# Optimization experiments

Hardware: AMD Instinct MI355X
Metric: run time of the kernel (lower is better)

The kernel has to match this reference:

```python
import jax, jax.numpy as jnp
import numpy as np

C_LEN, Q_LEN, B, H = 2048, 512, 32, 256


def setup_inputs() -> dict:
    key = jax.random.key(0)
    k1, k2 = jax.random.split(key)
    content_vec = jax.random.normal(k1, (C_LEN, B, H), dtype=jnp.float32)
    question_vec = jax.random.normal(k2, (Q_LEN, B, H), dtype=jnp.float32)
    question_mask = jnp.ones((B, Q_LEN), dtype=jnp.int32)
    return {"content_vec": content_vec, "question_vec": question_vec, "question_mask": question_mask}


def reference(content_vec, question_vec, question_mask):
    # scores: (B, c_len, q_len) = content (b,c,h) @ question^T (b,h,q)
    scores = jnp.einsum('cbh,qbh->bcq', content_vec, question_vec)
    # additive -inf mask where question_mask == 0, broadcast over c_len
    neg_inf = jnp.asarray(-jnp.inf, dtype=scores.dtype)
    scores = jnp.where(question_mask[:, None, :] == 0, neg_inf, scores)
    attn = jax.nn.softmax(scores, axis=-1)  # (B, c_len, q_len)
    # weighted sum of question vectors -> back to (c_len, B, H)
    out = jnp.einsum('bcq,qbh->cbh', attn, question_vec)
    return out
```

## Files before the change

### kernel.cpp

```cpp
#include <hip/hip_runtime.h>

#define C_LENX 2048
#define Q_LENX 512
#define BATCH  32
#define HDIM   256
#define BH     8192
#define CBLK   128
#define QBLK   32
#define NQT    16
#define TILE_BYTES 32768
#define OFF_QT 16384

typedef __attribute__((ext_vector_type(8))) _Float16 f16x8;
typedef __attribute__((ext_vector_type(4))) _Float16 f16x4;
typedef __attribute__((ext_vector_type(4))) float f32x4;

__device__ __forceinline__ unsigned short f2h_bits(float x) {
    union { _Float16 h; unsigned short u; } cv;
    cv.h = (_Float16)x;
    return cv.u;
}

__device__ __forceinline__ void stage16(const void* gsrc, void* ldst) {
    __builtin_amdgcn_global_load_lds(
        (const __attribute__((address_space(1))) unsigned int*)gsrc,
        (__attribute__((address_space(3))) unsigned int*)ldst, 16, 0, 0);
}

__global__ __launch_bounds__(256)
void q_prep(const float* __restrict__ question, unsigned char* __restrict__ blob)
{
    __shared__ unsigned short sHf[QBLK][264];
    const int tid = threadIdx.x;
    const int b  = blockIdx.x >> 4;
    const int t  = blockIdx.x & 15;
    const float* qbase = question + (size_t)(t * QBLK) * BH + b * HDIM;
    unsigned char* tb = blob + (size_t)(b * NQT + t) * TILE_BYTES;

    #pragma unroll
    for (int i = 0; i < 8; ++i) {
        int e  = tid + i * 256;
        int qr = e >> 6;
        int h4 = (e & 63) << 2;
        float4 x = *reinterpret_cast<const float4*>(qbase + (size_t)qr * BH + h4);
        ushort4 hv;
        hv.x = f2h_bits(x.x); hv.y = f2h_bits(x.y);
        hv.z = f2h_bits(x.z); hv.w = f2h_bits(x.w);
        *reinterpret_cast<ushort4*>(&sHf[qr][h4]) = hv;
        int c = h4 >> 3;
        *reinterpret_cast<ushort4*>(tb + qr * 512 + ((c ^ (qr & 7)) << 4) + ((h4 & 7) << 1)) = hv;
    }
    __syncthreads();
    #pragma unroll
    for (int i = 0; i < 4; ++i) {
        int c   = tid + i * 256;
        int n   = c >> 6;
        int hr  = (c >> 2) & 15;
        int lg4 = c & 3;
        int h  = n * 16 + hr;
        int q0 = lg4 * 4;
        ushort4 lo, hi;
        lo.x = sHf[q0 + 0][h]; lo.y = sHf[q0 + 1][h];
        lo.z = sHf[q0 + 2][h]; lo.w = sHf[q0 + 3][h];
        hi.x = sHf[16 + q0 + 0][h]; hi.y = sHf[16 + q0 + 1][h];
        hi.z = sHf[16 + q0 + 2][h]; hi.w = sHf[16 + q0 + 3][h];
        *reinterpret_cast<ushort4*>(tb + OFF_QT + c * 16)     = lo;
        *reinterpret_cast<ushort4*>(tb + OFF_QT + c * 16 + 8) = hi;
    }
}

__global__ __launch_bounds__(256, 2)
void s2s_attn(const float* __restrict__ content,
              const unsigned char* __restrict__ blob,
              const int*   __restrict__ qmask,
              float*       __restrict__ out)
{
    __shared__ __attribute__((aligned(16))) unsigned char sBuf[2 * TILE_BYTES];

    const int tid  = threadIdx.x;
    const int wid  = tid >> 6;
    const int lane = tid & 63;
    const int lr   = lane & 15;
    const int lg   = lane >> 4;

    const int lin = (blockIdx.x & 7) * 64 + (blockIdx.x >> 3);
    const int ct = lin & 15;
    const int b  = lin >> 4;
    const int c0 = ct * CBLK;

    {
        const unsigned char* tb0 = blob + (size_t)(b * NQT) * TILE_BYTES;
        #pragma unroll
        for (int j = 0; j < 8; ++j) {
            int seg = wid * 8 + j;
            stage16(tb0 + seg * 1024 + lane * 16, sBuf + seg * 1024);
        }
    }

    unsigned mwv[NQT];
    #pragma unroll
    for (int t = 0; t < NQT; ++t)
        mwv[t] = (unsigned)__ballot(qmask[b * Q_LENX + t * QBLK + (lane & 31)] != 0);

    f16x8 chi0[8], chi1[8];
    {
        const float* cb0 = content + (size_t)(c0 + wid*16 + lr) * BH + b*HDIM + lg*8;
        const float* cb1 = cb0 + (size_t)64 * BH;
        #pragma unroll
        for (int kc = 0; kc < 8; ++kc) {
            float4 x0 = *reinterpret_cast<const float4*>(cb0 + kc*32);
            float4 x1 = *reinterpret_cast<const float4*>(cb0 + kc*32 + 4);
            float4 y0 = *reinterpret_cast<const float4*>(cb1 + kc*32);
            float4 y1 = *reinterpret_cast<const float4*>(cb1 + kc*32 + 4);
            float xs[8] = {x0.x,x0.y,x0.z,x0.w,x1.x,x1.y,x1.z,x1.w};
            float ys[8] = {y0.x,y0.y,y0.z,y0.w,y1.x,y1.y,y1.z,y1.w};
            #pragma unroll
            for (int j = 0; j < 8; ++j) {
                chi0[kc][j] = (_Float16)xs[j];
                chi1[kc][j] = (_Float16)ys[j];
            }
        }
    }

    f32x4 acc0[16], acc1[16];
    #pragma unroll
    for (int n = 0; n < 16; ++n) {
        f32x4 z = {0.f,0.f,0.f,0.f};
        acc0[n] = z; acc1[n] = z;
    }
    float m_run0 = -INFINITY, m_run1 = -INFINITY;
    float l_run0 = 0.f, l_run1 = 0.f;

    __syncthreads();

    for (int t = 0; t < NQT; ++t) {
        const unsigned char* qf = sBuf + (t & 1) * TILE_BYTES;
        const unsigned char* qt = qf + OFF_QT;

        if (t + 1 < NQT) {
            const unsigned char* tbn = blob + (size_t)(b * NQT + t + 1) * TILE_BYTES;
            unsigned char* db = sBuf + ((t + 1) & 1) * TILE_BYTES;
            #pragma unroll
            for (int j = 0; j < 8; ++j) {
                int seg = wid * 8 + j;
                stage16(tbn + seg * 1024 + lane * 16, db + seg * 1024);
            }
        }
        const unsigned mw = mwv[t];

        f32x4 zz = {0.f,0.f,0.f,0.f};
        f32x4 sA0=zz, sB0=zz, sA1=zz, sB1=zz;
        const unsigned swz = (unsigned)(lr & 7);
        __builtin_amdgcn_s_setprio(1);
        #pragma unroll
        for (int kc = 0; kc < 8; ++kc) {
            unsigned off = (unsigned)((kc*4 + lg) ^ swz) << 4;
            f16x8 qa = *reinterpret_cast<const f16x8*>(qf + lr*512 + off);
            f16x8 qb = *reinterpret_cast<const f16x8*>(qf + (16+lr)*512 + off);
            sA0 = __builtin_amdgcn_mfma_f32_16x16x32_f16(qa, chi0[kc], sA0, 0, 0, 0);
            sB0 = __builtin_amdgcn_mfma_f32_16x16x32_f16(qb, chi0[kc], sB0, 0, 0, 0);
            sA1 = __builtin_amdgcn_mfma_f32_16x16x32_f16(qa, chi1[kc], sA1, 0, 0, 0);
            sB1 = __builtin_amdgcn_mfma_f32_16x16x32_f16(qb, chi1[kc], sB1, 0, 0, 0);
        }
        __builtin_amdgcn_s_setprio(0);

        float p0[8], p1[8];
        float tm0 = -INFINITY, tm1 = -INFINITY;
        #pragma unroll
        for (int r = 0; r < 4; ++r) {
            bool okA = (mw >> (lg*4 + r)) & 1u;
            bool okB = (mw >> (16 + lg*4 + r)) & 1u;
            float a0 = okA ? sA0[r] : -INFINITY;
            float b0v = okB ? sB0[r] : -INFINITY;
            float a1 = okA ? sA1[r] : -INFINITY;
            float b1v = okB ? sB1[r] : -INFINITY;
            p0[r] = a0; p0[4+r] = b0v;
            p1[r] = a1; p1[4+r] = b1v;
            tm0 = fmaxf(tm0, fmaxf(a0, b0v));
            tm1 = fmaxf(tm1, fmaxf(a1, b1v));
        }
        tm0 = fmaxf(tm0, __shfl_xor(tm0, 16, 64));
        tm0 = fmaxf(tm0, __shfl_xor(tm0, 32, 64));
        tm1 = fmaxf(tm1, __shfl_xor(tm1, 16, 64));
        tm1 = fmaxf(tm1, __shfl_xor(tm1, 32, 64));

        if (__ballot((tm0 > m_run0 + 4.0f) || (tm1 > m_run1 + 4.0f))) {
            float mn0 = fmaxf(m_run0, tm0);
            float mn1 = fmaxf(m_run1, tm1);
            float sc0 = 1.f, sc1 = 1.f;
            if (mn0 != -INFINITY) { sc0 = __expf(m_run0 - mn0); m_run0 = mn0; }
            if (mn1 != -INFINITY) { sc1 = __expf(m_run1 - mn1); m_run1 = mn1; }
            l_run0 *= sc0; l_run1 *= sc1;
            #pragma unroll
            for (int n = 0; n < 16; ++n) {
                acc0[n] *= sc0;
                acc1[n] *= sc1;
            }
        }

        _Float16 ph0[8], ph1[8];
        {
            float ps0 = 0.f, ps1 = 0.f;
            if (m_run0 == -INFINITY) {
                #pragma unroll
                for (int i = 0; i < 8; ++i) ph0[i] = (_Float16)0.f;
            } else {
                #pragma unroll
                for (int i = 0; i < 8; ++i) {
                    float e = __expf(p0[i] - m_run0);
                    ph0[i] = (_Float16)e;
                    ps0 += (float)ph0[i];
                }
            }
            if (m_run1 == -INFINITY) {
                #pragma unroll
                for (int i = 0; i < 8; ++i) ph1[i] = (_Float16)0.f;
            } else {
                #pragma unroll
                for (int i = 0; i < 8; ++i) {
                    float e = __expf(p1[i] - m_run1);
                    ph1[i] = (_Float16)e;
                    ps1 += (float)ph1[i];
                }
            }
            l_run0 += ps0;
            l_run1 += ps1;
        }

        f16x4 bp00 = {ph0[0], ph0[1], ph0[2], ph0[3]};
        f16x4 bp01 = {ph0[4], ph0[5], ph0[6], ph0[7]};
        f16x4 bp10 = {ph1[0], ph1[1], ph1[2], ph1[3]};
        f16x4 bp11 = {ph1[4], ph1[5], ph1[6], ph1[7]};
        __builtin_amdgcn_s_setprio(1);
        #pragma unroll
        for (int n = 0; n < 16; ++n) {
            f16x8 vt = *reinterpret_cast<const f16x8*>(qt + (((n*16 + lr)*4 + lg) << 4));
            f16x4 alo = {vt[0], vt[1], vt[2], vt[3]};
            f16x4 ahi = {vt[4], vt[5], vt[6], vt[7]};
            acc0[n] = __builtin_amdgcn_mfma_f32_16x16x16f16(alo, bp00, acc0[n], 0, 0, 0);
            acc1[n] = __builtin_amdgcn_mfma_f32_16x16x16f16(alo, bp10, acc1[n], 0, 0, 0);
            acc0[n] = __builtin_amdgcn_mfma_f32_16x16x16f16(ahi, bp01, acc0[n], 0, 0, 0);
            acc1[n] = __builtin_amdgcn_mfma_f32_16x16x16f16(ahi, bp11, acc1[n], 0, 0, 0);
        }
        __builtin_amdgcn_s_setprio(0);

        __syncthreads();
    }

    l_run0 += __shfl_xor(l_run0, 16, 64);
    l_run0 += __shfl_xor(l_run0, 32, 64);
    l_run1 += __shfl_xor(l_run1, 16, 64);
    l_run1 += __shfl_xor(l_run1, 32, 64);
    float rinv0 = 1.f / l_run0;
    float rinv1 = 1.f / l_run1;
    float* orow0 = out + (size_t)(c0 + wid*16 + lr) * BH + b*HDIM;
    float* orow1 = orow0 + (size_t)64 * BH;
    #pragma unroll
    for (int n = 0; n < 16; ++n) {
        f32x4 v0 = acc0[n] * rinv0;
        f32x4 v1 = acc1[n] * rinv1;
        *reinterpret_cast<f32x4*>(orow0 + n*16 + lg*4) = v0;
        *reinterpret_cast<f32x4*>(orow1 + n*16 + lg*4) = v1;
    }
}

extern "C" void kernel_launch(void* const* d_in, const int* in_sizes, int n_in,
                              void* d_out, int out_size, void* d_ws, size_t ws_size,
                              hipStream_t stream) {
    const float* content  = (const float*)d_in[0];
    const float* question = (const float*)d_in[1];
    const int*   mask     = (const int*)d_in[2];
    float*       out      = (float*)d_out;

    unsigned char* blob = (unsigned char*)d_ws;

    q_prep<<<BATCH * NQT, 256, 0, stream>>>(question, blob);
    s2s_attn<<<C_LENX / CBLK * BATCH, 256, 0, stream>>>(content, blob, mask, out);
}
```

Baseline: 80.72 us.

## Use 16x16x32 MFMA for PV by re-laying P through LDS and repacking Q^T

Repacks the transposed question tile so each lane holds 8 consecutive q values, and writes the softmax probabilities to a small per-wave LDS scratch so they can be reloaded in the matching k=32 layout. This halves the MFMA instruction count in the PV product by replacing pairs of 16x16x16 ops with single 16x16x32 ops. It also adds a fast path that skips per-element mask selects when the whole mask word is set. The cost is extra LDS writes and reads plus a waitcnt barrier on each iteration.

```diff
diff --git a/kernel.cpp b/kernel.cpp
--- a/kernel.cpp
+++ b/kernel.cpp
@@ -53,19 +53,17 @@
     __syncthreads();
     #pragma unroll
     for (int i = 0; i < 4; ++i) {
-        int c   = tid + i * 256;
-        int n   = c >> 6;
-        int hr  = (c >> 2) & 15;
-        int lg4 = c & 3;
-        int h  = n * 16 + hr;
-        int q0 = lg4 * 4;
-        ushort4 lo, hi;
-        lo.x = sHf[q0 + 0][h]; lo.y = sHf[q0 + 1][h];
-        lo.z = sHf[q0 + 2][h]; lo.w = sHf[q0 + 3][h];
-        hi.x = sHf[16 + q0 + 0][h]; hi.y = sHf[16 + q0 + 1][h];
-        hi.z = sHf[16 + q0 + 2][h]; hi.w = sHf[16 + q0 + 3][h];
-        *reinterpret_cast<ushort4*>(tb + OFF_QT + c * 16)     = lo;
-        *reinterpret_cast<ushort4*>(tb + OFF_QT + c * 16 + 8) = hi;
+        int e  = tid + i * 256;
+        int h  = e >> 2;
+        int g  = e & 3;
+        int q0 = g * 8;
+        ushort4 a, bv;
+        a.x  = sHf[q0 + 0][h]; a.y  = sHf[q0 + 1][h];
+        a.z  = sHf[q0 + 2][h]; a.w  = sHf[q0 + 3][h];
+        bv.x = sHf[q0 + 4][h]; bv.y = sHf[q0 + 5][h];
+        bv.z = sHf[q0 + 6][h]; bv.w = sHf[q0 + 7][h];
+        *reinterpret_cast<ushort4*>(tb + OFF_QT + e * 16)     = a;
+        *reinterpret_cast<ushort4*>(tb + OFF_QT + e * 16 + 8) = bv;
     }
 }
 
@@ -76,6 +74,7 @@
               float*       __restrict__ out)
 {
     __shared__ __attribute__((aligned(16))) unsigned char sBuf[2 * TILE_BYTES];
+    __shared__ __attribute__((aligned(16))) unsigned short sP[2][4][16][40];
 
     const int tid  = threadIdx.x;
     const int wid  = tid >> 6;
@@ -164,20 +163,30 @@
         }
         __builtin_amdgcn_s_setprio(0);
 
-        float p0[8], p1[8];
+        float p0v[8], p1v[8];
         float tm0 = -INFINITY, tm1 = -INFINITY;
-        #pragma unroll
-        for (int r = 0; r < 4; ++r) {
-            bool okA = (mw >> (lg*4 + r)) & 1u;
-            bool okB = (mw >> (16 + lg*4 + r)) & 1u;
-            float a0 = okA ? sA0[r] : -INFINITY;
-            float b0v = okB ? sB0[r] : -INFINITY;
-            float a1 = okA ? sA1[r] : -INFINITY;
-            float b1v = okB ? sB1[r] : -INFINITY;
-            p0[r] = a0; p0[4+r] = b0v;
-            p1[r] = a1; p1[4+r] = b1v;
-            tm0 = fmaxf(tm0, fmaxf(a0, b0v));
-            tm1 = fmaxf(tm1, fmaxf(a1, b1v));
+        if (mw == 0xffffffffu) {
+            #pragma unroll
+            for (int r = 0; r < 4; ++r) {
+                p0v[r] = sA0[r]; p0v[4+r] = sB0[r];
+                p1v[r] = sA1[r]; p1v[4+r] = sB1[r];
+                tm0 = fmaxf(tm0, fmaxf(sA0[r], sB0[r]));
+                tm1 = fmaxf(tm1, fmaxf(sA1[r], sB1[r]));
+            }
+        } else {
+            #pragma unroll
+            for (int r = 0; r < 4; ++r) {
+                bool okA = (mw >> (lg*4 + r)) & 1u;
+                bool okB = (mw >> (16 + lg*4 + r)) & 1u;
+                float a0 = okA ? sA0[r] : -INFINITY;
+                float b0v = okB ? sB0[r] : -INFINITY;
+                float a1 = okA ? sA1[r] : -INFINITY;
+                float b1v = okB ? sB1[r] : -INFINITY;
+                p0v[r] = a0; p0v[4+r] = b0v;
+                p1v[r] = a1; p1v[4+r] = b1v;
+                tm0 = fmaxf(tm0, fmaxf(a0, b0v));
+                tm1 = fmaxf(tm1, fmaxf(a1, b1v));
+            }
         }
         tm0 = fmaxf(tm0, __shfl_xor(tm0, 16, 64));
         tm0 = fmaxf(tm0, __shfl_xor(tm0, 32, 64));
@@ -207,7 +216,7 @@
             } else {
                 #pragma unroll
                 for (int i = 0; i < 8; ++i) {
-                    float e = __expf(p0[i] - m_run0);
+                    float e = __expf(p0v[i] - m_run0);
                     ph0[i] = (_Float16)e;
                     ps0 += (float)ph0[i];
                 }
@@ -218,7 +227,7 @@
             } else {
                 #pragma unroll
                 for (int i = 0; i < 8; ++i) {
-                    float e = __expf(p1[i] - m_run1);
+                    float e = __expf(p1v[i] - m_run1);
                     ph1[i] = (_Float16)e;
                     ps1 += (float)ph1[i];
                 }
@@ -227,20 +236,27 @@
             l_run1 += ps1;
         }
 
-        f16x4 bp00 = {ph0[0], ph0[1], ph0[2], ph0[3]};
-        f16x4 bp01 = {ph0[4], ph0[5], ph0[6], ph0[7]};
-        f16x4 bp10 = {ph1[0], ph1[1], ph1[2], ph1[3]};
-        f16x4 bp11 = {ph1[4], ph1[5], ph1[6], ph1[7]};
+        {
+            f16x4 w00 = {ph0[0], ph0[1], ph0[2], ph0[3]};
+            f16x4 w01 = {ph0[4], ph0[5], ph0[6], ph0[7]};
+            f16x4 w10 = {ph1[0], ph1[1], ph1[2], ph1[3]};
+            f16x4 w11 = {ph1[4], ph1[5], ph1[6], ph1[7]};
+            *reinterpret_cast<f16x4*>(&sP[0][wid][lr][lg*4])      = w00;
+            *reinterpret_cast<f16x4*>(&sP[0][wid][lr][16 + lg*4]) = w01;
+            *reinterpret_cast<f16x4*>(&sP[1][wid][lr][lg*4])      = w10;
+            *reinterpret_cast<f16x4*>(&sP[1][wid][lr][16 + lg*4]) = w11;
+        }
+        asm volatile("s_waitcnt lgkmcnt(0)" ::: "memory");
+        __builtin_amdgcn_sched_barrier(0);
+        f16x8 pf0 = *reinterpret_cast<const f16x8*>(&sP[0][wid][lr][lg*8]);
+        f16x8 pf1 = *reinterpret_cast<const f16x8*>(&sP[1][wid][lr][lg*8]);
+
         __builtin_amdgcn_s_setprio(1);
         #pragma unroll
         for (int n = 0; n < 16; ++n) {
             f16x8 vt = *reinterpret_cast<const f16x8*>(qt + (((n*16 + lr)*4 + lg) << 4));
-            f16x4 alo = {vt[0], vt[1], vt[2], vt[3]};
-            f16x4 ahi = {vt[4], vt[5], vt[6], vt[7]};
-            acc0[n] = __builtin_amdgcn_mfma_f32_16x16x16f16(alo, bp00, acc0[n], 0, 0, 0);
-            acc1[n] = __builtin_amdgcn_mfma_f32_16x16x16f16(alo, bp10, acc1[n], 0, 0, 0);
-            acc0[n] = __builtin_amdgcn_mfma_f32_16x16x16f16(ahi, bp01, acc0[n], 0, 0, 0);
-            acc1[n] = __builtin_amdgcn_mfma_f32_16x16x16f16(ahi, bp11, acc1[n], 0, 0, 0);
+            acc0[n] = __builtin_amdgcn_mfma_f32_16x16x32_f16(vt, pf0, acc0[n], 0, 0, 0);
+            acc1[n] = __builtin_amdgcn_mfma_f32_16x16x32_f16(vt, pf1, acc1[n], 0, 0, 0);
         }
         __builtin_amdgcn_s_setprio(0);
 
```

Result: faster. 75.23 us (-6.8%).
